# Kernel tuning notes

Hardware: AMD Instinct MI355X
Metric: run time of the kernel (lower is better)

The kernel has to match this reference:

```python
import jax, jax.numpy as jnp
import numpy as np

B, N, L = 1, 2048, 256
DX, DY, H = 1536, 768, 12
D = DX // H  # head_dim = 128
EPS_MOD = 1e-6   # modulated_rmsnorm eps
EPS_QK = 1e-5    # per-head RMSNorm eps


def setup_inputs() -> dict:
    key = jax.random.key(0)
    ks = jax.random.split(key, 16)
    def n(k, shape, s=1.0):
        return jax.random.normal(k, shape, dtype=jnp.float32) * s
    # rotary tables: (N, H, D//2), shared across heads
    pos = jnp.arange(N, dtype=jnp.float32)
    inv_freq = 1.0 / (10000.0 ** (jnp.arange(D // 2, dtype=jnp.float32) / (D // 2)))
    ang = pos[:, None] * inv_freq[None, :]                       # (N, D/2)
    rope_cos = jnp.broadcast_to(jnp.cos(ang)[:, None, :], (N, H, D // 2))
    rope_sin = jnp.broadcast_to(jnp.sin(ang)[:, None, :], (N, H, D // 2))
    return {
        "x": n(ks[0], (B, N, DX)),
        "y": n(ks[1], (B, L, DY)),
        "scale_x": n(ks[2], (B, DX), 0.1),
        "scale_y": n(ks[3], (B, DY), 0.1),
        "rope_cos": rope_cos,
        "rope_sin": rope_sin,
        "Wqkv_x": n(ks[4], (DX, 3 * DX), 0.02),
        "bqkv_x": jnp.zeros((3 * DX,), jnp.float32),
        "Wqkv_y": n(ks[5], (DY, 3 * DX), 0.02),
        "bqkv_y": jnp.zeros((3 * DX,), jnp.float32),
        "q_norm_x_w": jnp.ones((D,), jnp.float32),
        "k_norm_x_w": jnp.ones((D,), jnp.float32),
        "q_norm_y_w": jnp.ones((D,), jnp.float32),
        "k_norm_y_w": jnp.ones((D,), jnp.float32),
        "Wproj_x": n(ks[6], (DX, DX), 0.02),
        "bproj_x": jnp.zeros((DX,), jnp.float32),
        "Wproj_y": n(ks[7], (DX, DY), 0.02),
        "bproj_y": jnp.zeros((DY,), jnp.float32),
    }


def _rms(v, eps):
    return v * jax.lax.rsqrt(jnp.mean(v * v, axis=-1, keepdims=True) + eps)


def _rope(q, cos, sin):
    # q: (B, S, H, D); cos/sin: (S, H, D/2); even/odd interleaved rotation
    qe, qo = q[..., 0::2], q[..., 1::2]
    re = qe * cos - qo * sin
    ro = qe * sin + qo * cos
    return jnp.stack([re, ro], axis=-1).reshape(q.shape)


def reference(x, y, scale_x, scale_y, rope_cos, rope_sin,
              Wqkv_x, bqkv_x, Wqkv_y, bqkv_y,
              q_norm_x_w, k_norm_x_w, q_norm_y_w, k_norm_y_w,
              Wproj_x, bproj_x, Wproj_y, bproj_y):
    b, n, dx = x.shape
    _, l, _ = y.shape
    h, d = H, D
    # --- visual stream ---
    xm = _rms(x, EPS_MOD) * (1.0 + scale_x[:, None, :])          # modulated_rmsnorm
    qkv = (xm @ Wqkv_x + bqkv_x).reshape(b, n, 3, h, d)
    q_x, k_x, v_x = qkv[:, :, 0], qkv[:, :, 1], qkv[:, :, 2]
    q_x = _rope(_rms(q_x, EPS_QK) * q_norm_x_w, rope_cos, rope_sin)
    k_x = _rope(_rms(k_x, EPS_QK) * k_norm_x_w, rope_cos, rope_sin)
    # --- text stream ---
    ym = _rms(y, EPS_MOD) * (1.0 + scale_y[:, None, :])
    qkvy = (ym @ Wqkv_y + bqkv_y).reshape(b, l, 3, h, d)
    q_y, k_y, v_y = qkvy[:, :, 0], qkvy[:, :, 1], qkvy[:, :, 2]
    q_y = _rms(q_y, EPS_QK) * q_norm_y_w
    k_y = _rms(k_y, EPS_QK) * k_norm_y_w
    # --- joint attention over concatenated sequence (B, H, N+L, D) ---
    q = jnp.concatenate([q_x, q_y], axis=1).transpose(0, 2, 1, 3)
    k = jnp.concatenate([k_x, k_y], axis=1).transpose(0, 2, 1, 3)
    v = jnp.concatenate([v_x, v_y], axis=1).transpose(0, 2, 1, 3)
    scale = 1.0 / np.sqrt(d).astype(np.float32)
    attn = jax.nn.softmax(jnp.einsum('bhqd,bhkd->bhqk', q, k) * scale, axis=-1)
    out = jnp.einsum('bhqk,bhkd->bhqd', attn, v)
    out = out.transpose(0, 2, 1, 3).reshape(b, n + l, h * d)
    x_out = out[:, :n] @ Wproj_x + bproj_x
    y_out = out[:, n:] @ Wproj_y + bproj_y
    return (x_out, y_out)
```

## Files before the change

### kernel.cpp

```cpp
#include <hip/hip_runtime.h>

typedef unsigned short u16;
typedef __attribute__((ext_vector_type(8))) short short8;
typedef __attribute__((ext_vector_type(4))) short short4v;
typedef __attribute__((ext_vector_type(4))) float floatx4;

__device__ __forceinline__ u16 f2bf(float f) {
  return (u16)((__float_as_uint(f) + 0x8000u) >> 16);
}
__device__ __forceinline__ float bf2f(u16 v) {
  return __uint_as_float(((unsigned)v) << 16);
}
__device__ __forceinline__ unsigned cvt_pk_bf16(float a, float b) {
  unsigned r;
  asm("v_cvt_pk_bf16_f32 %0, %1, %2" : "=v"(r) : "v"(a), "v"(b));
  return r;
}

#define GLD16(g, l) __builtin_amdgcn_global_load_lds( \
    (const __attribute__((address_space(1))) void*)(g), \
    (__attribute__((address_space(3))) void*)(l), 16, 0, 0)

__global__ __launch_bounds__(256) void prep(const float* __restrict__ W0, u16* __restrict__ T0,
                                            const float* __restrict__ W1, u16* __restrict__ T1,
                                            const float* __restrict__ W2, u16* __restrict__ T2,
                                            const float* __restrict__ W3, u16* __restrict__ T3,
                                            const float* __restrict__ x, const float* __restrict__ scale_x,
                                            const float* __restrict__ y, const float* __restrict__ scale_y,
                                            u16* __restrict__ xm, u16* __restrict__ ym) {
  __shared__ float t[32][33];
  const int z = blockIdx.z;
  if (z < 4) {
    const float* in; u16* out; int K, N;
    switch (z) {
      case 0: in = W0; out = T0; K = 1536; N = 4608; break;
      case 1: in = W1; out = T1; K = 768;  N = 4608; break;
      case 2: in = W2; out = T2; K = 1536; N = 1536; break;
      default: in = W3; out = T3; K = 1536; N = 768; break;
    }
    const int n0 = blockIdx.x * 32, k0 = blockIdx.y * 32;
    if (n0 >= N || k0 >= K) return;
    const int tx = threadIdx.x, ty = threadIdx.y;
#pragma unroll
    for (int i = 0; i < 32; i += 8)
      t[ty + i][tx] = in[(size_t)(k0 + ty + i) * N + n0 + tx];
    __syncthreads();
#pragma unroll
    for (int i = 0; i < 32; i += 8)
      out[(size_t)(n0 + ty + i) * K + k0 + tx] = f2bf(t[tx][ty + i]);
  } else {
    const int row = blockIdx.y * 144 + blockIdx.x;
    if (row >= 2304) return;
    const int tid = threadIdx.y * 32 + threadIdx.x;
    const float* xr; const float* sc; u16* dst; int D;
    if (row < 2048) { D = 1536; xr = x + (size_t)row * D; sc = scale_x; dst = xm + (size_t)row * D; }
    else { D = 768; xr = y + (size_t)(row - 2048) * D; sc = scale_y; dst = ym + (size_t)(row - 2048) * D; }
    float ss = 0.f;
    for (int c = tid; c < D; c += 256) { float v = xr[c]; ss += v * v; }
    for (int off = 32; off > 0; off >>= 1) ss += __shfl_down(ss, off);
    __shared__ float red[4];
    if ((tid & 63) == 0) red[tid >> 6] = ss;
    __syncthreads();
    const float tot = red[0] + red[1] + red[2] + red[3];
    const float r = rsqrtf(tot / (float)D + 1e-6f);
    for (int c = tid; c < D; c += 256)
      dst[c] = f2bf(xr[c] * r * (1.0f + sc[c]));
  }
}

template <bool BOUT>
__global__ __launch_bounds__(256) void gemm2(const u16* __restrict__ A0, const u16* __restrict__ BT0,
                                             const float* __restrict__ bias0, void* __restrict__ C0,
                                             int M0, int N0, int K0,
                                             const u16* __restrict__ A1, const u16* __restrict__ BT1,
                                             const float* __restrict__ bias1, void* __restrict__ C1,
                                             int M1, int N1, int K1) {
  const u16 *A, *BT; const float* bias; void* Cout; int M, N, K;
  if (blockIdx.z == 0) { A = A0; BT = BT0; bias = bias0; Cout = C0; M = M0; N = N0; K = K0; }
  else { A = A1; BT = BT1; bias = bias1; Cout = C1; M = M1; N = N1; K = K1; }
  const int bm = blockIdx.y * 128, bn = blockIdx.x * 128;
  if (bm >= M || bn >= N) return;

  __shared__ __align__(16) u16 As[128 * 32];
  __shared__ __align__(16) u16 Bs[128 * 32];
  const int tid = threadIdx.x;
  const int lane = tid & 63, wave = tid >> 6;
  const int wm = (wave & 1) * 64, wn = (wave >> 1) * 64;
  const int row16 = lane & 15, quad = lane >> 4;

  floatx4 acc[4][4] = {};
  const int r0 = lane >> 2, c4 = (lane & 3) * 8;
  const u16* Ag0 = A + (size_t)(bm + wave * 16 + r0) * K + c4;
  const u16* Ag1 = A + (size_t)(bm + (wave + 4) * 16 + r0) * K + c4;
  const u16* Bg0 = BT + (size_t)(bn + wave * 16 + r0) * K + c4;
  const u16* Bg1 = BT + (size_t)(bn + (wave + 4) * 16 + r0) * K + c4;
  u16* As0 = As + wave * 512; u16* As1 = As + (wave + 4) * 512;
  u16* Bs0 = Bs + wave * 512; u16* Bs1 = Bs + (wave + 4) * 512;

  for (int k0 = 0; k0 < K; k0 += 32) {
    GLD16(Ag0 + k0, As0);
    GLD16(Ag1 + k0, As1);
    GLD16(Bg0 + k0, Bs0);
    GLD16(Bg1 + k0, Bs1);
    __syncthreads();
    short8 af[4], bf[4];
#pragma unroll
    for (int i = 0; i < 4; i++) {
      af[i] = *(const short8*)&As[(wm + i * 16 + row16) * 32 + quad * 8];
      bf[i] = *(const short8*)&Bs[(wn + i * 16 + row16) * 32 + quad * 8];
    }
#pragma unroll
    for (int mi = 0; mi < 4; mi++)
#pragma unroll
      for (int ni = 0; ni < 4; ni++)
        acc[mi][ni] = __builtin_amdgcn_mfma_f32_16x16x32_bf16(af[mi], bf[ni], acc[mi][ni], 0, 0, 0);
    __syncthreads();
  }
#pragma unroll
  for (int mi = 0; mi < 4; mi++) {
#pragma unroll
    for (int ni = 0; ni < 4; ni++) {
      const int col = bn + wn + ni * 16 + row16;
      const float b = bias[col];
      const int row0 = bm + wm + mi * 16 + quad * 4;
#pragma unroll
      for (int r = 0; r < 4; r++) {
        const float v = acc[mi][ni][r] + b;
        if constexpr (BOUT)
          ((u16*)Cout)[(size_t)(row0 + r) * N + col] = f2bf(v);
        else
          ((float*)Cout)[(size_t)(row0 + r) * N + col] = v;
      }
    }
  }
}

__global__ __launch_bounds__(128) void qkv_post(const u16* __restrict__ qkvx,
                                                const u16* __restrict__ qkvy,
                                                const float* __restrict__ qnwx, const float* __restrict__ knwx,
                                                const float* __restrict__ qnwy, const float* __restrict__ knwy,
                                                const float* __restrict__ rcos, const float* __restrict__ rsin,
                                                u16* __restrict__ Q, u16* __restrict__ Kb, u16* __restrict__ V) {
  const int s = blockIdx.x, h = blockIdx.y, d = threadIdx.x;
  const bool isx = s < 2048;
  const u16* base = isx ? (qkvx + (size_t)s * 4608) : (qkvy + (size_t)(s - 2048) * 4608);
  const float q = bf2f(base[h * 128 + d]);
  const float k = bf2f(base[1536 + h * 128 + d]);
  const u16 v = base[3072 + h * 128 + d];
  __shared__ float redq[2], redk[2];
  float sq = q * q, sk = k * k;
  for (int off = 32; off > 0; off >>= 1) { sq += __shfl_down(sq, off); sk += __shfl_down(sk, off); }
  const int lane = threadIdx.x & 63, w = threadIdx.x >> 6;
  if (lane == 0) { redq[w] = sq; redk[w] = sk; }
  __syncthreads();
  const float rq = rsqrtf((redq[0] + redq[1]) * (1.f / 128.f) + 1e-5f);
  const float rk = rsqrtf((redk[0] + redk[1]) * (1.f / 128.f) + 1e-5f);
  float qn = q * rq * (isx ? qnwx[d] : qnwy[d]);
  float kn = k * rk * (isx ? knwx[d] : knwy[d]);
  if (isx) {
    const int i = d >> 1;
    const float c = rcos[((size_t)s * 12 + h) * 64 + i];
    const float sn = rsin[((size_t)s * 12 + h) * 64 + i];
    const float qo = __shfl_xor(qn, 1);
    const float ko = __shfl_xor(kn, 1);
    qn = (d & 1) ? (qo * sn + qn * c) : (qn * c - qo * sn);
    kn = (d & 1) ? (ko * sn + kn * c) : (kn * c - ko * sn);
  }
  qn *= 0.12751737942f;
  const size_t o = ((size_t)h * 2304 + s) * 128 + d;
  Q[o] = f2bf(qn);
  Kb[o] = f2bf(kn);
  V[o] = v;
}

__global__ __launch_bounds__(256) void vtrans(const u16* __restrict__ V, u16* __restrict__ Vt) {
  __shared__ u16 t[32][33];
  const int h = blockIdx.x, st = blockIdx.y * 32, dt = blockIdx.z * 32;
  const u16* Vh = V + (size_t)h * 2304 * 128;
  u16* Vth = Vt + (size_t)h * 128 * 2304;
  const int tx = threadIdx.x, ty = threadIdx.y;
#pragma unroll
  for (int i = 0; i < 32; i += 8)
    t[ty + i][tx] = Vh[(size_t)(st + ty + i) * 128 + dt + tx];
  __syncthreads();
#pragma unroll
  for (int i = 0; i < 32; i += 8)
    Vth[(size_t)(dt + ty + i) * 2304 + st + tx] = t[tx][ty + i];
}

__global__ __launch_bounds__(256, 3) void attn(const u16* __restrict__ Q, const u16* __restrict__ Kb,
                                               const u16* __restrict__ Vt,
                                               u16* __restrict__ Opart,
                                               float* __restrict__ Mp, float* __restrict__ Lp) {
  const int bid = blockIdx.x;
  const int xcd = bid & 7, local = bid >> 3;
  const int combo = xcd * 6 + local / 18;
  const int qt = local % 18;
  const int h = combo % 12, split = combo / 12;
  const int q0 = qt * 128;
  const int tid = threadIdx.x, lane = tid & 63, wave = tid >> 6;
  const int row16 = lane & 15, quad = lane >> 4;
  const u16* Qh = Q + (size_t)h * 2304 * 128;
  const u16* Kh = Kb + (size_t)h * 2304 * 128;
  const u16* Vh = Vt + (size_t)h * 128 * 2304;

  __shared__ __align__(16) u16 Ks[64 * 128];
  __shared__ __align__(16) u16 Vs[128 * 64];
  __shared__ __align__(16) u16 Ps[4][32 * 64];

  short8 qf[2][4];
#pragma unroll
  for (int g = 0; g < 2; g++) {
    const u16* qrow = Qh + (size_t)(q0 + wave * 32 + g * 16 + row16) * 128;
#pragma unroll
    for (int kk = 0; kk < 4; kk++) qf[g][kk] = *(const short8*)(qrow + kk * 32 + quad * 8);
  }
  floatx4 oacc[2][8] = {};
  float m_i[2] = {-1e30f, -1e30f}, l_i[2] = {0.f, 0.f};

  const u16* Kp[4]; const u16* Vp[4];
#pragma unroll
  for (int i = 0; i < 4; i++) {
    const int j = i * 4 + wave;
    const int krow = j * 4 + (lane >> 4);
    const int kcol = ((lane & 15) ^ (krow & 7)) * 8;
    const int vrow = j * 8 + (lane >> 3);
    const int vcol = ((lane & 7) ^ (vrow & 7)) * 8;
    Kp[i] = Kh + (size_t)krow * 128 + kcol;
    Vp[i] = Vh + (size_t)vrow * 2304 + vcol;
  }
  const int sw = row16 & 7;
  const int kbeg = split * 576, kend = kbeg + 576;

  for (int kt = kbeg; kt < kend; kt += 64) {
    __syncthreads();
#pragma unroll
    for (int i = 0; i < 4; i++) {
      GLD16(Kp[i] + (size_t)kt * 128, Ks + (i * 4 + wave) * 512);
      GLD16(Vp[i] + kt, Vs + (i * 4 + wave) * 512);
    }
    __syncthreads();

    floatx4 sacc[2][4] = {};
#pragma unroll
    for (int mk = 0; mk < 4; mk++) {
#pragma unroll
      for (int kk = 0; kk < 4; kk++) {
        const int c = (4 * kk + quad) ^ sw;
        const short8 kfrag = *(const short8*)&Ks[(mk * 16 + row16) * 128 + c * 8];
        sacc[0][mk] = __builtin_amdgcn_mfma_f32_16x16x32_bf16(kfrag, qf[0][kk], sacc[0][mk], 0, 0, 0);
        sacc[1][mk] = __builtin_amdgcn_mfma_f32_16x16x32_bf16(kfrag, qf[1][kk], sacc[1][mk], 0, 0, 0);
      }
    }
#pragma unroll
    for (int g = 0; g < 2; g++) {
      float mx = sacc[g][0][0];
#pragma unroll
      for (int mk = 0; mk < 4; mk++)
#pragma unroll
        for (int r = 0; r < 4; r++) mx = fmaxf(mx, sacc[g][mk][r]);
      mx = fmaxf(mx, __shfl_xor(mx, 16));
      mx = fmaxf(mx, __shfl_xor(mx, 32));
      if (__any(mx > m_i[g] + 8.f)) {
        const float mnew = fmaxf(m_i[g], mx);
        const float alpha = __builtin_amdgcn_exp2f(m_i[g] - mnew);
        m_i[g] = mnew;
        const float a0 = __shfl(alpha, quad * 4 + 0);
        const float a1 = __shfl(alpha, quad * 4 + 1);
        const float a2 = __shfl(alpha, quad * 4 + 2);
        const float a3 = __shfl(alpha, quad * 4 + 3);
#pragma unroll
        for (int nd = 0; nd < 8; nd++) {
          oacc[g][nd][0] *= a0; oacc[g][nd][1] *= a1; oacc[g][nd][2] *= a2; oacc[g][nd][3] *= a3;
        }
        l_i[g] *= alpha;
      }
      float s = 0.f;
#pragma unroll
      for (int mk = 0; mk < 4; mk++)
#pragma unroll
        for (int r = 0; r < 4; r++) {
          const float p = __builtin_amdgcn_exp2f(sacc[g][mk][r] - m_i[g]);
          sacc[g][mk][r] = p;
          s += p;
        }
      s += __shfl_xor(s, 16);
      s += __shfl_xor(s, 32);
      l_i[g] += s;
    }

#pragma unroll
    for (int g = 0; g < 2; g++)
#pragma unroll
      for (int mk = 0; mk < 4; mk++) {
        const int subp = (4 * mk + quad) ^ (sw << 1);
        uint2 pk;
        pk.x = cvt_pk_bf16(sacc[g][mk][0], sacc[g][mk][1]);
        pk.y = cvt_pk_bf16(sacc[g][mk][2], sacc[g][mk][3]);
        *(uint2*)&Ps[wave][(g * 16 + row16) * 64 + subp * 4] = pk;
      }
    const int pc0 = quad ^ sw, pc1 = (4 + quad) ^ sw;
    short8 pf[2][2];
#pragma unroll
    for (int g = 0; g < 2; g++) {
      pf[g][0] = *(const short8*)&Ps[wave][(g * 16 + row16) * 64 + pc0 * 8];
      pf[g][1] = *(const short8*)&Ps[wave][(g * 16 + row16) * 64 + pc1 * 8];
    }
#pragma unroll
    for (int nd = 0; nd < 8; nd++) {
      const short8 vf0 = *(const short8*)&Vs[(nd * 16 + row16) * 64 + pc0 * 8];
      const short8 vf1 = *(const short8*)&Vs[(nd * 16 + row16) * 64 + pc1 * 8];
      oacc[0][nd] = __builtin_amdgcn_mfma_f32_16x16x32_bf16(pf[0][0], vf0, oacc[0][nd], 0, 0, 0);
      oacc[0][nd] = __builtin_amdgcn_mfma_f32_16x16x32_bf16(pf[0][1], vf1, oacc[0][nd], 0, 0, 0);
      oacc[1][nd] = __builtin_amdgcn_mfma_f32_16x16x32_bf16(pf[1][0], vf0, oacc[1][nd], 0, 0, 0);
      oacc[1][nd] = __builtin_amdgcn_mfma_f32_16x16x32_bf16(pf[1][1], vf1, oacc[1][nd], 0, 0, 0);
    }
  }
#pragma unroll
  for (int g = 0; g < 2; g++) {
    const size_t base = (size_t)(split * 12 + h) * 2304 + q0 + wave * 32 + g * 16;
#pragma unroll
    for (int nd = 0; nd < 8; nd++)
#pragma unroll
      for (int r = 0; r < 4; r++)
        Opart[(base + quad * 4 + r) * 128 + nd * 16 + row16] = f2bf(oacc[g][nd][r]);
    if (lane < 16) { Mp[base + lane] = m_i[g]; Lp[base + lane] = l_i[g]; }
  }
}

__global__ __launch_bounds__(256) void attn_combine(const u16* __restrict__ Opart,
                                                    const float* __restrict__ Mp,
                                                    const float* __restrict__ Lp,
                                                    u16* __restrict__ attnout) {
  const int idx = blockIdx.x * 256 + threadIdx.x;
  const int dd = (idx & 31) * 4;
  const int hq = idx >> 5;
  const int h = hq % 12, q = hq / 12;
  size_t b[4]; float ms[4], ls[4];
  float m = -1e30f;
#pragma unroll
  for (int s = 0; s < 4; s++) {
    b[s] = (size_t)(s * 12 + h) * 2304 + q;
    ms[s] = Mp[b[s]]; ls[s] = Lp[b[s]];
    m = fmaxf(m, ms[s]);
  }
  float w[4], denom = 0.f;
#pragma unroll
  for (int s = 0; s < 4; s++) { w[s] = exp2f(ms[s] - m); denom += ls[s] * w[s]; }
  const float inv = 1.0f / denom;
  float ox = 0.f, oy = 0.f, oz = 0.f, ow = 0.f;
#pragma unroll
  for (int s = 0; s < 4; s++) {
    const short4v o = *(const short4v*)&Opart[b[s] * 128 + dd];
    ox += bf2f((u16)o[0]) * w[s]; oy += bf2f((u16)o[1]) * w[s];
    oz += bf2f((u16)o[2]) * w[s]; ow += bf2f((u16)o[3]) * w[s];
  }
  short4v out;
  out[0] = (short)f2bf(ox * inv);
  out[1] = (short)f2bf(oy * inv);
  out[2] = (short)f2bf(oz * inv);
  out[3] = (short)f2bf(ow * inv);
  *(short4v*)&attnout[(size_t)idx * 4] = out;
}

extern "C" void kernel_launch(void* const* d_in, const int* in_sizes, int n_in,
                              void* d_out, int out_size, void* d_ws, size_t ws_size,
                              hipStream_t stream) {
  const float* x        = (const float*)d_in[0];
  const float* y        = (const float*)d_in[1];
  const float* scale_x  = (const float*)d_in[2];
  const float* scale_y  = (const float*)d_in[3];
  const float* rope_cos = (const float*)d_in[4];
  const float* rope_sin = (const float*)d_in[5];
  const float* Wqkv_x   = (const float*)d_in[6];
  const float* bqkv_x   = (const float*)d_in[7];
  const float* Wqkv_y   = (const float*)d_in[8];
  const float* bqkv_y   = (const float*)d_in[9];
  const float* qnwx     = (const float*)d_in[10];
  const float* knwx     = (const float*)d_in[11];
  const float* qnwy     = (const float*)d_in[12];
  const float* knwy     = (const float*)d_in[13];
  const float* Wproj_x  = (const float*)d_in[14];
  const float* bproj_x  = (const float*)d_in[15];
  const float* Wproj_y  = (const float*)d_in[16];
  const float* bproj_y  = (const float*)d_in[17];
  float* out = (float*)d_out;

  char* ws = (char*)d_ws;
  size_t off = 0;
  auto take = [&](size_t bytes) { char* p = ws + off; off += (bytes + 255) & ~(size_t)255; return p; };
  u16* WqkvxT  = (u16*)take((size_t)4608 * 1536 * 2);
  u16* WqkvyT  = (u16*)take((size_t)4608 * 768 * 2);
  u16* WprojxT = (u16*)take((size_t)1536 * 1536 * 2);
  u16* WprojyT = (u16*)take((size_t)768 * 1536 * 2);
  u16* xm      = (u16*)take((size_t)2048 * 1536 * 2);
  u16* ym      = (u16*)take((size_t)256 * 768 * 2);
  u16* qkvx    = (u16*)take((size_t)2048 * 4608 * 2);
  u16* qkvy    = (u16*)take((size_t)256 * 4608 * 2);
  u16* Qb      = (u16*)take((size_t)12 * 2304 * 128 * 2);
  u16* Kb      = (u16*)take((size_t)12 * 2304 * 128 * 2);
  u16* Vb      = (u16*)take((size_t)12 * 2304 * 128 * 2);
  u16* Vt      = (u16*)take((size_t)12 * 128 * 2304 * 2);
  u16* attnout = (u16*)take((size_t)2304 * 1536 * 2);
  u16* Opart   = (u16*)take((size_t)4 * 12 * 2304 * 128 * 2);
  float* Mp    = (float*)take((size_t)4 * 12 * 2304 * 4);
  float* Lp    = (float*)take((size_t)4 * 12 * 2304 * 4);

  prep<<<dim3(144, 48, 5), dim3(32, 8), 0, stream>>>(Wqkv_x, WqkvxT, Wqkv_y, WqkvyT,
                                                     Wproj_x, WprojxT, Wproj_y, WprojyT,
                                                     x, scale_x, y, scale_y, xm, ym);

  gemm2<true><<<dim3(36, 16, 2), 256, 0, stream>>>(xm, WqkvxT, bqkv_x, qkvx, 2048, 4608, 1536,
                                                   ym, WqkvyT, bqkv_y, qkvy, 256, 4608, 768);

  qkv_post<<<dim3(2304, 12), 128, 0, stream>>>(qkvx, qkvy, qnwx, knwx, qnwy, knwy,
                                               rope_cos, rope_sin, Qb, Kb, Vb);
  vtrans<<<dim3(12, 2304 / 32, 128 / 32), dim3(32, 8), 0, stream>>>(Vb, Vt);

  attn<<<dim3(864), 256, 0, stream>>>(Qb, Kb, Vt, Opart, Mp, Lp);
  attn_combine<<<(2304 * 1536 / 4) / 256, 256, 0, stream>>>(Opart, Mp, Lp, attnout);

  gemm2<false><<<dim3(12, 16, 2), 256, 0, stream>>>(attnout, WprojxT, bproj_x, out, 2048, 1536, 1536,
                                                    attnout + (size_t)2048 * 1536, WprojyT, bproj_y,
                                                    out + (size_t)2048 * 1536, 256, 768, 1536);
  (void)in_sizes; (void)n_in; (void)out_size; (void)ws_size;
}
```

Baseline: 331.3 us.

## Prefetch next K/V tile into registers during attention compute, shrink P buffer

Replaces the synchronous global_load_lds K/V staging with register prefetch: the next tile's K and V are loaded into registers while the current tile's QK^T, softmax and PV run, then written to LDS after a barrier. The per-wave P scratch is halved by reusing one 16-row buffer for both row groups, and launch bounds are raised to 4 blocks per CU. This is meant to hide global load latency and raise occupancy, at the cost of extra VGPRs for the prefetch registers under a tighter register budget, which may cause spills.

```diff
diff --git a/kernel.cpp b/kernel.cpp
--- a/kernel.cpp
+++ b/kernel.cpp
@@ -188,7 +188,7 @@
     Vth[(size_t)(dt + ty + i) * 2304 + st + tx] = t[tx][ty + i];
 }
 
-__global__ __launch_bounds__(256, 3) void attn(const u16* __restrict__ Q, const u16* __restrict__ Kb,
+__global__ __launch_bounds__(256, 4) void attn(const u16* __restrict__ Q, const u16* __restrict__ Kb,
                                                const u16* __restrict__ Vt,
                                                u16* __restrict__ Opart,
                                                float* __restrict__ Mp, float* __restrict__ Lp) {
@@ -206,7 +206,7 @@
 
   __shared__ __align__(16) u16 Ks[64 * 128];
   __shared__ __align__(16) u16 Vs[128 * 64];
-  __shared__ __align__(16) u16 Ps[4][32 * 64];
+  __shared__ __align__(16) u16 Ps[4][16 * 64];
 
   short8 qf[2][4];
 #pragma unroll
@@ -219,6 +219,7 @@
   float m_i[2] = {-1e30f, -1e30f}, l_i[2] = {0.f, 0.f};
 
   const u16* Kp[4]; const u16* Vp[4];
+  int kds[4], vds[4];
 #pragma unroll
   for (int i = 0; i < 4; i++) {
     const int j = i * 4 + wave;
@@ -228,18 +229,35 @@
     const int vcol = ((lane & 7) ^ (vrow & 7)) * 8;
     Kp[i] = Kh + (size_t)krow * 128 + kcol;
     Vp[i] = Vh + (size_t)vrow * 2304 + vcol;
+    kds[i] = j * 512 + lane * 8;
+    vds[i] = j * 512 + lane * 8;
   }
   const int sw = row16 & 7;
   const int kbeg = split * 576, kend = kbeg + 576;
 
+  typedef __attribute__((ext_vector_type(4))) unsigned uint4v;
+  uint4v kreg[4], vreg[4];
+#pragma unroll
+  for (int i = 0; i < 4; i++) {
+    kreg[i] = *(const uint4v*)(Kp[i] + (size_t)kbeg * 128);
+    vreg[i] = *(const uint4v*)(Vp[i] + kbeg);
+  }
+#pragma unroll
+  for (int i = 0; i < 4; i++) {
+    *(uint4v*)&Ks[kds[i]] = kreg[i];
+    *(uint4v*)&Vs[vds[i]] = vreg[i];
+  }
+  __syncthreads();
+
   for (int kt = kbeg; kt < kend; kt += 64) {
-    __syncthreads();
-#pragma unroll
-    for (int i = 0; i < 4; i++) {
-      GLD16(Kp[i] + (size_t)kt * 128, Ks + (i * 4 + wave) * 512);
-      GLD16(Vp[i] + kt, Vs + (i * 4 + wave) * 512);
-    }
-    __syncthreads();
+    const bool more = (kt + 64) < kend;
+    if (more) {
+#pragma unroll
+      for (int i = 0; i < 4; i++) {
+        kreg[i] = *(const uint4v*)(Kp[i] + (size_t)(kt + 64) * 128);
+        vreg[i] = *(const uint4v*)(Vp[i] + (kt + 64));
+      }
+    }
 
     floatx4 sacc[2][4] = {};
 #pragma unroll
@@ -289,22 +307,20 @@
       l_i[g] += s;
     }
 
-#pragma unroll
-    for (int g = 0; g < 2; g++)
+    const int pc0 = quad ^ sw, pc1 = (4 + quad) ^ sw;
+    short8 pf[2][2];
+#pragma unroll
+    for (int g = 0; g < 2; g++) {
 #pragma unroll
       for (int mk = 0; mk < 4; mk++) {
         const int subp = (4 * mk + quad) ^ (sw << 1);
         uint2 pk;
         pk.x = cvt_pk_bf16(sacc[g][mk][0], sacc[g][mk][1]);
         pk.y = cvt_pk_bf16(sacc[g][mk][2], sacc[g][mk][3]);
-        *(uint2*)&Ps[wave][(g * 16 + row16) * 64 + subp * 4] = pk;
-      }
-    const int pc0 = quad ^ sw, pc1 = (4 + quad) ^ sw;
-    short8 pf[2][2];
-#pragma unroll
-    for (int g = 0; g < 2; g++) {
-      pf[g][0] = *(const short8*)&Ps[wave][(g * 16 + row16) * 64 + pc0 * 8];
-      pf[g][1] = *(const short8*)&Ps[wave][(g * 16 + row16) * 64 + pc1 * 8];
+        *(uint2*)&Ps[wave][row16 * 64 + subp * 4] = pk;
+      }
+      pf[g][0] = *(const short8*)&Ps[wave][row16 * 64 + pc0 * 8];
+      pf[g][1] = *(const short8*)&Ps[wave][row16 * 64 + pc1 * 8];
     }
 #pragma unroll
     for (int nd = 0; nd < 8; nd++) {
@@ -314,6 +330,16 @@
       oacc[0][nd] = __builtin_amdgcn_mfma_f32_16x16x32_bf16(pf[0][1], vf1, oacc[0][nd], 0, 0, 0);
       oacc[1][nd] = __builtin_amdgcn_mfma_f32_16x16x32_bf16(pf[1][0], vf0, oacc[1][nd], 0, 0, 0);
       oacc[1][nd] = __builtin_amdgcn_mfma_f32_16x16x32_bf16(pf[1][1], vf1, oacc[1][nd], 0, 0, 0);
+    }
+
+    __syncthreads();
+    if (more) {
+#pragma unroll
+      for (int i = 0; i < 4; i++) {
+        *(uint4v*)&Ks[kds[i]] = kreg[i];
+        *(uint4v*)&Vs[vds[i]] = vreg[i];
+      }
+      __syncthreads();
     }
   }
 #pragma unroll
```

After: 474.8 us. 43.3% more time.

## Double-buffer LDS tiles in gemm2 to overlap global loads with MFMA

Applied to the files above, without the earlier changes.

Gives gemm2 two LDS buffers for the A and B tiles and prefetches the next K-slice with global_load_lds while the current slice goes through MFMA. Manual vmcnt waits plus raw s_barrier replace the two __syncthreads per iteration. The goal is to hide global memory latency behind compute. In exchange LDS use doubles, and correctness now depends on the hand-written waitcnt ordering and on the compiler not reordering LDS reads across the barriers.

```diff
diff --git a/kernel.cpp b/kernel.cpp
--- a/kernel.cpp
+++ b/kernel.cpp
@@ -81,8 +81,8 @@
   const int bm = blockIdx.y * 128, bn = blockIdx.x * 128;
   if (bm >= M || bn >= N) return;
 
-  __shared__ __align__(16) u16 As[128 * 32];
-  __shared__ __align__(16) u16 Bs[128 * 32];
+  __shared__ __align__(16) u16 As[2][128 * 32];
+  __shared__ __align__(16) u16 Bs[2][128 * 32];
   const int tid = threadIdx.x;
   const int lane = tid & 63, wave = tid >> 6;
   const int wm = (wave & 1) * 64, wn = (wave >> 1) * 64;
@@ -94,27 +94,40 @@
   const u16* Ag1 = A + (size_t)(bm + (wave + 4) * 16 + r0) * K + c4;
   const u16* Bg0 = BT + (size_t)(bn + wave * 16 + r0) * K + c4;
   const u16* Bg1 = BT + (size_t)(bn + (wave + 4) * 16 + r0) * K + c4;
-  u16* As0 = As + wave * 512; u16* As1 = As + (wave + 4) * 512;
-  u16* Bs0 = Bs + wave * 512; u16* Bs1 = Bs + (wave + 4) * 512;
-
+  const int d0 = wave * 512, d1 = (wave + 4) * 512;
+
+  GLD16(Ag0, &As[0][d0]);
+  GLD16(Ag1, &As[0][d1]);
+  GLD16(Bg0, &Bs[0][d0]);
+  GLD16(Bg1, &Bs[0][d1]);
+
+  int cur = 0;
   for (int k0 = 0; k0 < K; k0 += 32) {
-    GLD16(Ag0 + k0, As0);
-    GLD16(Ag1 + k0, As1);
-    GLD16(Bg0 + k0, Bs0);
-    GLD16(Bg1 + k0, Bs1);
-    __syncthreads();
+    if (k0 + 32 < K) {
+      GLD16(Ag0 + k0 + 32, &As[cur ^ 1][d0]);
+      GLD16(Ag1 + k0 + 32, &As[cur ^ 1][d1]);
+      GLD16(Bg0 + k0 + 32, &Bs[cur ^ 1][d0]);
+      GLD16(Bg1 + k0 + 32, &Bs[cur ^ 1][d1]);
+      asm volatile("s_waitcnt vmcnt(4)" ::: "memory");
+    } else {
+      asm volatile("s_waitcnt vmcnt(0)" ::: "memory");
+    }
+    __builtin_amdgcn_s_barrier();
+    asm volatile("" ::: "memory");
     short8 af[4], bf[4];
 #pragma unroll
     for (int i = 0; i < 4; i++) {
-      af[i] = *(const short8*)&As[(wm + i * 16 + row16) * 32 + quad * 8];
-      bf[i] = *(const short8*)&Bs[(wn + i * 16 + row16) * 32 + quad * 8];
+      af[i] = *(const short8*)&As[cur][(wm + i * 16 + row16) * 32 + quad * 8];
+      bf[i] = *(const short8*)&Bs[cur][(wn + i * 16 + row16) * 32 + quad * 8];
     }
 #pragma unroll
     for (int mi = 0; mi < 4; mi++)
 #pragma unroll
       for (int ni = 0; ni < 4; ni++)
         acc[mi][ni] = __builtin_amdgcn_mfma_f32_16x16x32_bf16(af[mi], bf[ni], acc[mi][ni], 0, 0, 0);
-    __syncthreads();
+    asm volatile("" ::: "memory");
+    __builtin_amdgcn_s_barrier();
+    cur ^= 1;
   }
 #pragma unroll
   for (int mi = 0; mi < 4; mi++) {
```

New measurement: 317.7 us. 1.04x faster.
